# Performance work log

Measured on AMD Instinct MI355X. Metric: run time of the kernel, lower is better.

Reference implementation:

```python
import jax, jax.numpy as jnp
import numpy as np

B, N, H, HEADS = 4, 4096, 256, 8
DEG = 16
E = B * N * DEG  # 262144 edges
DH = H // HEADS


def setup_inputs() -> dict:
    key = jax.random.key(0)
    ks = jax.random.split(key, 8)
    node_states = jax.random.normal(ks[0], (B, N, H), dtype=jnp.float32)
    # edge_indices rows: [batch_idx, target_node, source_node]
    b_idx = jnp.repeat(jnp.arange(B, dtype=jnp.int64), N * DEG)
    tgt = jnp.tile(jnp.repeat(jnp.arange(N, dtype=jnp.int64), DEG), B)
    src = jax.random.randint(ks[1], (E,), 0, N, dtype=jnp.int64)
    edge_indices = jnp.stack([b_idx, tgt, src])  # (3, E)
    s = 1.0 / np.sqrt(H)
    Wq = jax.random.normal(ks[2], (H, H), dtype=jnp.float32) * s
    Wk = jax.random.normal(ks[3], (H, H), dtype=jnp.float32) * s
    Wv = jax.random.normal(ks[4], (H, H), dtype=jnp.float32) * s
    bq = jnp.zeros((H,), dtype=jnp.float32)
    bk = jnp.zeros((H,), dtype=jnp.float32)
    bv = jnp.zeros((H,), dtype=jnp.float32)
    return {"node_states": node_states, "edge_indices": edge_indices,
            "Wq": Wq, "bq": bq, "Wk": Wk, "bk": bk, "Wv": Wv, "bv": bv}


def reference(node_states, edge_indices, Wq, bq, Wk, bk, Wv, bv):
    batch, n_nodes, hidden = node_states.shape
    b_idx, tgt, src = edge_indices[0], edge_indices[1], edge_indices[2]
    num_edges = b_idx.shape[0]

    # Dense Q/K/V projections on nodes (cheap), then per-edge gathers.
    Q = (node_states @ Wq + bq).reshape(batch, n_nodes, HEADS, DH)
    K = (node_states @ Wk + bk).reshape(batch, n_nodes, HEADS, DH)
    V = (node_states @ Wv + bv).reshape(batch, n_nodes, HEADS, DH)

    q_e = Q[b_idx, tgt]  # (E, heads, dh)
    k_e = K[b_idx, src]  # (E, heads, dh)
    scores = jnp.sum(q_e * k_e, axis=-1) / jnp.sqrt(jnp.float32(DH))  # (E, heads)

    # Segment softmax over source nodes, grouped per (batch, target) --
    # mirrors torch.sparse.softmax(logits, dim=-2).
    seg = b_idx * n_nodes + tgt  # (E,)
    num_seg = batch * n_nodes
    m = jax.ops.segment_max(scores, seg, num_segments=num_seg)  # (B*N, heads)
    exp = jnp.exp(scores - m[seg])
    denom = jax.ops.segment_sum(exp, seg, num_segments=num_seg)
    attn = exp / denom[seg]  # (E, heads)

    # Weighted scatter-sum of source values into target nodes
    # (replaces sparse edge_mask @ elwise_prod).
    v_e = V[b_idx, src]  # (E, heads, dh)
    weighted = (attn[..., None] * v_e).reshape(num_edges, hidden)
    out = jax.ops.segment_sum(weighted, seg, num_segments=num_seg)
    return out.reshape(batch, n_nodes, hidden)
```

## Files before the change

kernel.cpp:

```cpp
#include <hip/hip_runtime.h>
#include <hip/hip_bf16.h>

#define BATCH 4
#define NNODES 4096
#define HID 256
#define NHEADS 8
#define DH 32
#define DEG 16
#define NEDGES (BATCH * NNODES * DEG)
#define NROWS (BATCH * NNODES)

typedef __attribute__((ext_vector_type(8))) short short8;
typedef __attribute__((ext_vector_type(8))) unsigned short ushort8;
typedef __attribute__((ext_vector_type(4))) unsigned short u16x4;
typedef __attribute__((ext_vector_type(4))) float f32x4;

static __device__ __forceinline__ unsigned short f2bf(float f) {
  __hip_bfloat16 h = __float2bfloat16(f);
  return *reinterpret_cast<unsigned short*>(&h);
}
static __device__ __forceinline__ float bf2f(unsigned short u) {
  unsigned int v = ((unsigned int)u) << 16;
  return *reinterpret_cast<float*>(&v);
}

__global__ __launch_bounds__(256, 4) void qkv_mfma_kernel(
    const float* __restrict__ X,
    const float* __restrict__ Wq, const float* __restrict__ Wk,
    const float* __restrict__ Wv,
    const float* __restrict__ bq, const float* __restrict__ bk,
    const float* __restrict__ bv,
    float* __restrict__ Qs, unsigned short* __restrict__ Kb,
    unsigned short* __restrict__ Vb) {
  __shared__ unsigned short sW[16384];

  const int tid = threadIdx.x;
  const int xcd = blockIdx.x & 7;
  const int l = blockIdx.x >> 3;
  const int s = l % 12;
  const int chunk = (l / 12) * 8 + xcd;
  const int mat = s >> 2;
  const int c0 = (s & 3) * 64;
  const float* __restrict__ W = (mat == 0) ? Wq : (mat == 1) ? Wk : Wv;

  #pragma unroll
  for (int i = 0; i < 8; ++i) {
    const int hi_s = tid >> 6;
    const int col = tid & 63;
    const int k0 = i * 32 + hi_s * 8;
    ushort8 o;
    #pragma unroll
    for (int j = 0; j < 8; ++j) {
      o[j] = f2bf(W[(size_t)(k0 + j) * HID + c0 + col]);
    }
    *reinterpret_cast<ushort8*>(&sW[(i * 256 + tid) * 8]) = o;
  }

  const int lane = tid & 63;
  const int wv = tid >> 6;
  const int lm = lane & 15;
  const int hi = lane >> 4;
  const int lk = hi * 8;
  const int row = chunk * 64 + wv * 16 + lm;

  short8 Af[8];
  #pragma unroll
  for (int kk = 0; kk < 8; ++kk) {
    const float4 a0 = *reinterpret_cast<const float4*>(&X[(size_t)row * 256 + kk * 32 + lk]);
    const float4 a1 = *reinterpret_cast<const float4*>(&X[(size_t)row * 256 + kk * 32 + lk + 4]);
    short8 v;
    v[0] = (short)f2bf(a0.x); v[1] = (short)f2bf(a0.y);
    v[2] = (short)f2bf(a0.z); v[3] = (short)f2bf(a0.w);
    v[4] = (short)f2bf(a1.x); v[5] = (short)f2bf(a1.y);
    v[6] = (short)f2bf(a1.z); v[7] = (short)f2bf(a1.w);
    Af[kk] = v;
  }

  const float* __restrict__ bias = (mat == 0) ? bq : (mat == 1) ? bk : bv;

  __syncthreads();

  #pragma unroll
  for (int nt = 0; nt < 4; ++nt) {
    short8 Bf[8];
    #pragma unroll
    for (int kk = 0; kk < 8; ++kk) {
      Bf[kk] = *reinterpret_cast<const short8*>(
          &sW[kk * 2048 + hi * 512 + (nt * 16 + lm) * 8]);
    }
    f32x4 acc = {0.f, 0.f, 0.f, 0.f};
    #pragma unroll
    for (int kk = 0; kk < 8; ++kk) {
      acc = __builtin_amdgcn_mfma_f32_16x16x32_bf16(Bf[kk], Af[kk], acc, 0, 0, 0);
    }
    const int col0 = c0 + nt * 16 + hi * 4;
    const float4 b4 = *reinterpret_cast<const float4*>(&bias[col0]);
    if (mat == 0) {
      float4 o;
      o.x = acc[0] + b4.x; o.y = acc[1] + b4.y;
      o.z = acc[2] + b4.z; o.w = acc[3] + b4.w;
      *reinterpret_cast<float4*>(&Qs[(size_t)row * 256 + col0]) = o;
    } else {
      u16x4 o;
      o[0] = f2bf(acc[0] + b4.x); o[1] = f2bf(acc[1] + b4.y);
      o[2] = f2bf(acc[2] + b4.z); o[3] = f2bf(acc[3] + b4.w);
      unsigned short* __restrict__ dst = (mat == 1) ? Kb : Vb;
      *reinterpret_cast<u16x4*>(&dst[(size_t)row * 256 + col0]) = o;
    }
  }
}

__global__ __launch_bounds__(256) void attn_kernel(
    const float* __restrict__ Q, const unsigned short* __restrict__ K,
    const unsigned short* __restrict__ V, const int* __restrict__ edges,
    float* __restrict__ out) {
  __shared__ float s_w[DEG * NHEADS];

  const int bx = blockIdx.x;
  const int xcd = bx & 7;
  const int g = (xcd >> 1) * NNODES + (((bx >> 3) << 1) | (xcd & 1));
  const int e0 = g * DEG;
  const int tid = threadIdx.x;

  const int b = edges[e0];
  const int qrow = b * NNODES + edges[NEDGES + e0];

  const int lane = tid & 63;
  const int wv = tid >> 6;
  const int j = lane >> 2;
  const int hh = (lane >> 1) & 1;
  const int p = lane & 1;
  const int h = wv * 2 + hh;
  const int ch0 = h * 32 + p * 16;

  const int nsrc = b * NNODES + edges[2 * NEDGES + e0 + j];

  const float* __restrict__ qp = &Q[(size_t)qrow * HID + ch0];
  const float4 q0 = *reinterpret_cast<const float4*>(qp);
  const float4 q1 = *reinterpret_cast<const float4*>(qp + 4);
  const float4 q2 = *reinterpret_cast<const float4*>(qp + 8);
  const float4 q3 = *reinterpret_cast<const float4*>(qp + 12);
  const unsigned short* __restrict__ kp = &K[(size_t)nsrc * HID + ch0];
  const ushort8 k0 = *reinterpret_cast<const ushort8*>(kp);
  const ushort8 k1 = *reinterpret_cast<const ushort8*>(kp + 8);

  float partial;
  partial  = q0.x * bf2f(k0[0]); partial = fmaf(q0.y, bf2f(k0[1]), partial);
  partial = fmaf(q0.z, bf2f(k0[2]), partial); partial = fmaf(q0.w, bf2f(k0[3]), partial);
  partial = fmaf(q1.x, bf2f(k0[4]), partial); partial = fmaf(q1.y, bf2f(k0[5]), partial);
  partial = fmaf(q1.z, bf2f(k0[6]), partial); partial = fmaf(q1.w, bf2f(k0[7]), partial);
  partial = fmaf(q2.x, bf2f(k1[0]), partial); partial = fmaf(q2.y, bf2f(k1[1]), partial);
  partial = fmaf(q2.z, bf2f(k1[2]), partial); partial = fmaf(q2.w, bf2f(k1[3]), partial);
  partial = fmaf(q3.x, bf2f(k1[4]), partial); partial = fmaf(q3.y, bf2f(k1[5]), partial);
  partial = fmaf(q3.z, bf2f(k1[6]), partial); partial = fmaf(q3.w, bf2f(k1[7]), partial);

  partial += __shfl_xor(partial, 1);
  const float sc = partial * 0.17677669529663687f;

  float mx = sc;
  mx = fmaxf(mx, __shfl_xor(mx, 4));
  mx = fmaxf(mx, __shfl_xor(mx, 8));
  mx = fmaxf(mx, __shfl_xor(mx, 16));
  mx = fmaxf(mx, __shfl_xor(mx, 32));
  const float e = __expf(sc - mx);
  float sum = e;
  sum += __shfl_xor(sum, 4);
  sum += __shfl_xor(sum, 8);
  sum += __shfl_xor(sum, 16);
  sum += __shfl_xor(sum, 32);

  if (p == 0) s_w[j * NHEADS + h] = e / sum;
  __syncthreads();

  const int h3 = tid >> 5;
  float acc = 0.0f;
  #pragma unroll
  for (int jj = 0; jj < DEG; ++jj) {
    const int n = b * NNODES + edges[2 * NEDGES + e0 + jj];
    acc = fmaf(s_w[jj * NHEADS + h3], bf2f(V[(size_t)n * HID + tid]), acc);
  }
  out[(size_t)qrow * HID + tid] = acc;
}

extern "C" void kernel_launch(void* const* d_in, const int* in_sizes, int n_in,
                              void* d_out, int out_size, void* d_ws, size_t ws_size,
                              hipStream_t stream) {
  const float* X     = (const float*)d_in[0];
  const int*   edges = (const int*)d_in[1];
  const float* Wq    = (const float*)d_in[2];
  const float* bq    = (const float*)d_in[3];
  const float* Wk    = (const float*)d_in[4];
  const float* bk    = (const float*)d_in[5];
  const float* Wv    = (const float*)d_in[6];
  const float* bv    = (const float*)d_in[7];
  float* out = (float*)d_out;

  char* w = (char*)d_ws;
  float*          Qs = (float*)w;                 w += (size_t)NROWS * HID * 4;
  unsigned short* Kb = (unsigned short*)w;        w += (size_t)NROWS * HID * 2;
  unsigned short* Vb = (unsigned short*)w;

  qkv_mfma_kernel<<<3072, 256, 0, stream>>>(X, Wq, Wk, Wv, bq, bk, bv, Qs, Kb, Vb);
  attn_kernel<<<NROWS, 256, 0, stream>>>(Qs, Kb, Vb, edges, out);
}
```

Measured before the change: 70.18 us.

## Pre-convert weights to bf16 once and reuse X fragments across Q/K/V

Adds a small prep kernel that converts Wq/Wk/Wv to bf16 in the MFMA-friendly shared-memory layout once, so each QKV block just copies pre-laid-out tiles instead of doing strided fp32 loads and conversions. Each block now loops over all three matrices for a 64-column strip, reusing the converted X fragments in registers and cutting the grid from 3072 to 1024 blocks. This removes redundant X reads/conversions and per-block weight conversion, at the cost of an extra kernel launch and less parallelism per block.

After: 63.38 us. -9.7%, faster.

```diff
diff --git a/kernel.cpp b/kernel.cpp
--- a/kernel.cpp
+++ b/kernel.cpp
@@ -24,10 +24,30 @@
   return *reinterpret_cast<float*>(&v);
 }
 
+__global__ __launch_bounds__(256) void w_prep_kernel(
+    const float* __restrict__ Wq, const float* __restrict__ Wk,
+    const float* __restrict__ Wv, unsigned short* __restrict__ Wt) {
+  const int o = blockIdx.x * 2048 + threadIdx.x * 8;
+  const int mat   = o >> 16;
+  const int w     = o & 65535;
+  const int strip = w >> 14;
+  const int r     = w & 16383;
+  const int kk    = r >> 11;
+  const int hi    = (r >> 9) & 3;
+  const int col   = (r >> 3) & 63;
+  const int k0    = kk * 32 + hi * 8;
+  const int c     = strip * 64 + col;
+  const float* __restrict__ W = (mat == 0) ? Wq : (mat == 1) ? Wk : Wv;
+  ushort8 ovec;
+  #pragma unroll
+  for (int j = 0; j < 8; ++j) {
+    ovec[j] = f2bf(W[(size_t)(k0 + j) * HID + c]);
+  }
+  *reinterpret_cast<ushort8*>(&Wt[o]) = ovec;
+}
+
 __global__ __launch_bounds__(256, 4) void qkv_mfma_kernel(
-    const float* __restrict__ X,
-    const float* __restrict__ Wq, const float* __restrict__ Wk,
-    const float* __restrict__ Wv,
+    const float* __restrict__ X, const unsigned short* __restrict__ Wt,
     const float* __restrict__ bq, const float* __restrict__ bk,
     const float* __restrict__ bv,
     float* __restrict__ Qs, unsigned short* __restrict__ Kb,
@@ -37,24 +57,9 @@
   const int tid = threadIdx.x;
   const int xcd = blockIdx.x & 7;
   const int l = blockIdx.x >> 3;
-  const int s = l % 12;
-  const int chunk = (l / 12) * 8 + xcd;
-  const int mat = s >> 2;
-  const int c0 = (s & 3) * 64;
-  const float* __restrict__ W = (mat == 0) ? Wq : (mat == 1) ? Wk : Wv;
-
-  #pragma unroll
-  for (int i = 0; i < 8; ++i) {
-    const int hi_s = tid >> 6;
-    const int col = tid & 63;
-    const int k0 = i * 32 + hi_s * 8;
-    ushort8 o;
-    #pragma unroll
-    for (int j = 0; j < 8; ++j) {
-      o[j] = f2bf(W[(size_t)(k0 + j) * HID + c0 + col]);
-    }
-    *reinterpret_cast<ushort8*>(&sW[(i * 256 + tid) * 8]) = o;
-  }
+  const int cs = l & 3;
+  const int chunk = (l >> 2) * 8 + xcd;
+  const int c0 = cs * 64;
 
   const int lane = tid & 63;
   const int wv = tid >> 6;
@@ -76,37 +81,48 @@
     Af[kk] = v;
   }
 
-  const float* __restrict__ bias = (mat == 0) ? bq : (mat == 1) ? bk : bv;
-
-  __syncthreads();
-
-  #pragma unroll
-  for (int nt = 0; nt < 4; ++nt) {
-    short8 Bf[8];
+  #pragma unroll
+  for (int m = 0; m < 3; ++m) {
+    const unsigned short* __restrict__ Wsrc = Wt + (size_t)(m * 4 + cs) * 16384;
     #pragma unroll
-    for (int kk = 0; kk < 8; ++kk) {
-      Bf[kk] = *reinterpret_cast<const short8*>(
-          &sW[kk * 2048 + hi * 512 + (nt * 16 + lm) * 8]);
+    for (int i = 0; i < 8; ++i) {
+      const int e = i * 2048 + tid * 8;
+      *reinterpret_cast<ushort8*>(&sW[e]) =
+          *reinterpret_cast<const ushort8*>(&Wsrc[e]);
     }
-    f32x4 acc = {0.f, 0.f, 0.f, 0.f};
+    __syncthreads();
+
+    const float* __restrict__ bias = (m == 0) ? bq : (m == 1) ? bk : bv;
+
     #pragma unroll
-    for (int kk = 0; kk < 8; ++kk) {
-      acc = __builtin_amdgcn_mfma_f32_16x16x32_bf16(Bf[kk], Af[kk], acc, 0, 0, 0);
+    for (int nt = 0; nt < 4; ++nt) {
+      short8 Bf[8];
+      #pragma unroll
+      for (int kk = 0; kk < 8; ++kk) {
+        Bf[kk] = *reinterpret_cast<const short8*>(
+            &sW[kk * 2048 + hi * 512 + (nt * 16 + lm) * 8]);
+      }
+      f32x4 acc = {0.f, 0.f, 0.f, 0.f};
+      #pragma unroll
+      for (int kk = 0; kk < 8; ++kk) {
+        acc = __builtin_amdgcn_mfma_f32_16x16x32_bf16(Bf[kk], Af[kk], acc, 0, 0, 0);
+      }
+      const int col0 = c0 + nt * 16 + hi * 4;
+      const float4 b4 = *reinterpret_cast<const float4*>(&bias[col0]);
+      if (m == 0) {
+        float4 o;
+        o.x = acc[0] + b4.x; o.y = acc[1] + b4.y;
+        o.z = acc[2] + b4.z; o.w = acc[3] + b4.w;
+        *reinterpret_cast<float4*>(&Qs[(size_t)row * 256 + col0]) = o;
+      } else {
+        u16x4 o;
+        o[0] = f2bf(acc[0] + b4.x); o[1] = f2bf(acc[1] + b4.y);
+        o[2] = f2bf(acc[2] + b4.z); o[3] = f2bf(acc[3] + b4.w);
+        unsigned short* __restrict__ dst = (m == 1) ? Kb : Vb;
+        *reinterpret_cast<u16x4*>(&dst[(size_t)row * 256 + col0]) = o;
+      }
     }
-    const int col0 = c0 + nt * 16 + hi * 4;
-    const float4 b4 = *reinterpret_cast<const float4*>(&bias[col0]);
-    if (mat == 0) {
-      float4 o;
-      o.x = acc[0] + b4.x; o.y = acc[1] + b4.y;
-      o.z = acc[2] + b4.z; o.w = acc[3] + b4.w;
-      *reinterpret_cast<float4*>(&Qs[(size_t)row * 256 + col0]) = o;
-    } else {
-      u16x4 o;
-      o[0] = f2bf(acc[0] + b4.x); o[1] = f2bf(acc[1] + b4.y);
-      o[2] = f2bf(acc[2] + b4.z); o[3] = f2bf(acc[3] + b4.w);
-      unsigned short* __restrict__ dst = (mat == 1) ? Kb : Vb;
-      *reinterpret_cast<u16x4*>(&dst[(size_t)row * 256 + col0]) = o;
-    }
+    __syncthreads();
   }
 }
 
@@ -198,8 +214,10 @@
   char* w = (char*)d_ws;
   float*          Qs = (float*)w;                 w += (size_t)NROWS * HID * 4;
   unsigned short* Kb = (unsigned short*)w;        w += (size_t)NROWS * HID * 2;
-  unsigned short* Vb = (unsigned short*)w;
-
-  qkv_mfma_kernel<<<3072, 256, 0, stream>>>(X, Wq, Wk, Wv, bq, bk, bv, Qs, Kb, Vb);
+  unsigned short* Vb = (unsigned short*)w;        w += (size_t)NROWS * HID * 2;
+  unsigned short* Wt = (unsigned short*)w;
+
+  w_prep_kernel<<<96, 256, 0, stream>>>(Wq, Wk, Wv, Wt);
+  qkv_mfma_kernel<<<1024, 256, 0, stream>>>(X, Wt, bq, bk, bv, Qs, Kb, Vb);
   attn_kernel<<<NROWS, 256, 0, stream>>>(Qs, Kb, Vb, edges, out);
 }
```
